# Performance work log

Hardware: AMD Instinct MI355X
Metric: run time of the kernel (lower is better)

## Reference

```python
import jax, jax.numpy as jnp
import numpy as np

DIM = 512
HID = 2048
L = 4
VOCAB = 32000
EPS = 1e-6
B, S = 2, 2048


def rmsnorm(x, w, eps=EPS):
    xf = x.astype(jnp.float32)
    n = xf * jax.lax.rsqrt(jnp.mean(xf * xf, axis=-1, keepdims=True) + eps)
    return n.astype(x.dtype) * w


def setup_inputs() -> dict:
    key = jax.random.key(0)
    ks = jax.random.split(key, 12)
    sd = 0.02
    tokens = jax.random.randint(ks[0], (B, S), 0, VOCAB)
    emb = jax.random.normal(ks[1], (VOCAB, DIM), jnp.float32) * sd  # tied out_proj.weight
    decay_norm_w = jnp.ones((L, DIM), jnp.float32)
    lambda_w = jax.random.normal(ks[2], (L, 1, DIM), jnp.float32) * sd
    quantity_w = jax.random.normal(ks[3], (L, DIM, DIM), jnp.float32) * sd
    gate_w = jax.random.normal(ks[4], (L, DIM, DIM), jnp.float32) * sd
    output_w = jax.random.normal(ks[5], (L, DIM, DIM), jnp.float32) * sd
    ffn_norm_w = jnp.ones((L, DIM), jnp.float32)
    w_h = jax.random.normal(ks[6], (L, HID, DIM), jnp.float32) * sd
    w_g = jax.random.normal(ks[7], (L, HID, DIM), jnp.float32) * sd
    w_o = jax.random.normal(ks[8], (L, DIM, HID), jnp.float32) * sd
    out_norm_w = jnp.ones((DIM,), jnp.float32)
    return dict(tokens=tokens, emb=emb, decay_norm_w=decay_norm_w, lambda_w=lambda_w,
                quantity_w=quantity_w, gate_w=gate_w, output_w=output_w,
                ffn_norm_w=ffn_norm_w, w_h=w_h, w_g=w_g, w_o=w_o, out_norm_w=out_norm_w)


def _ted_forward(tokens, emb, decay_norm_w, lambda_w, quantity_w, gate_w,
                 output_w, ffn_norm_w, w_h, w_g, w_o, out_norm_w):
    s = tokens.shape[-1]
    idx = jnp.arange(s, dtype=jnp.float32)
    # time[i,j] = relu(i - j) ; equivalent to ones.tril_(-1).cumsum_(-2)
    time = jnp.maximum(idx[:, None] - idx[None, :], 0.0)  # [S,S]
    causal = idx[:, None] >= idx[None, :]                 # tril mask incl. diag
    x = emb[tokens]  # [B,S,D]
    for l in range(L):
        h = rmsnorm(x, decay_norm_w[l])
        # negative lambdas: log(sigmoid(h @ W_l^T)) -> [B,S,1] -> [B,1,S]
        nl = jnp.swapaxes(jax.nn.log_sigmoid(h @ lambda_w[l].T), -1, -2)
        decay = jnp.where(causal, jnp.exp(nl * time), 0.0)  # [B,S,S]
        q = h @ quantity_w[l].T                             # [B,S,D]
        out = jnp.einsum('bst,btd->bsd', decay, q)
        x = x + (jax.nn.silu(out) @ output_w[l].T) * (h @ gate_w[l].T)
        f = rmsnorm(x, ffn_norm_w[l])
        x = x + ((f @ w_h[l].T) * jax.nn.silu(f @ w_g[l].T)) @ w_o[l].T
    return rmsnorm(x, out_norm_w) @ emb.T  # [B,S,V]


def reference(tokens, emb, decay_norm_w, lambda_w, quantity_w, gate_w,
              output_w, ffn_norm_w, w_h, w_g, w_o, out_norm_w):
    return _ted_forward(tokens, emb, decay_norm_w, lambda_w, quantity_w, gate_w,
                        output_w, ffn_norm_w, w_h, w_g, w_o, out_norm_w)
```

## Files before the change

### kernel.cpp

```cpp
#include <hip/hip_runtime.h>
#include <cstdint>
#include <cstddef>


typedef __bf16 bf16_t;
typedef __bf16 bf16x2 __attribute__((ext_vector_type(2)));
typedef __bf16 bf16x4 __attribute__((ext_vector_type(4)));
typedef __bf16 bf16x8 __attribute__((ext_vector_type(8)));
typedef float  f32x4  __attribute__((ext_vector_type(4)));

#define TED_DIM   512
#define TED_HID   2048
#define TED_L     4
#define TED_VOCAB 32000
#define TED_B     2
#define TED_S     2048
#define TED_ROWS  4096
#define LOG2E     1.44269504088896340736f

#define GLDS16(gp, lp)                                                  \
    __builtin_amdgcn_global_load_lds(                                   \
        (__attribute__((address_space(1))) void*)(gp),                  \
        (__attribute__((address_space(3))) void*)(lp), 16, 0, 0)

__global__ void cvt_kernel(const float* __restrict__ in, bf16_t* __restrict__ out, int n4)
{
    int i = blockIdx.x * blockDim.x + threadIdx.x;
    if (i < n4) {
        float4 v = ((const float4*)in)[i];
        bf16x4 o;
        o[0] = (bf16_t)v.x; o[1] = (bf16_t)v.y; o[2] = (bf16_t)v.z; o[3] = (bf16_t)v.w;
        ((bf16x4*)out)[i] = o;
    }
}

__global__ void embed_kernel(const int* __restrict__ tok, const float* __restrict__ emb,
                             float* __restrict__ x)
{
    int r = blockIdx.x;
    int t = threadIdx.x;
    int id = tok[r];
    float4 v = *(const float4*)&emb[(size_t)id * TED_DIM + t * 4];
    *(float4*)&x[(size_t)r * TED_DIM + t * 4] = v;
}

__global__ void rmsnorm_kernel(const float* __restrict__ x, const float* __restrict__ w,
                               const float* __restrict__ lam,
                               bf16_t* __restrict__ hout, float* __restrict__ nl2out)
{
    int row = blockIdx.x;
    int t = threadIdx.x;
    int lane = t & 63, wv = t >> 6;
    const float* xr = x + (size_t)row * TED_DIM;

    float2 v = *(const float2*)&xr[t * 2];
    float ss = v.x * v.x + v.y * v.y;
    #pragma unroll
    for (int off = 32; off; off >>= 1) ss += __shfl_down(ss, off, 64);

    __shared__ float red[4];
    __shared__ float sscale;
    if (lane == 0) red[wv] = ss;
    __syncthreads();
    if (t == 0) {
        float s = red[0] + red[1] + red[2] + red[3];
        sscale = rsqrtf(s * (1.0f / (float)TED_DIM) + 1e-6f);
    }
    __syncthreads();
    float scale = sscale;

    float2 wv2 = *(const float2*)&w[t * 2];
    float h0 = v.x * scale * wv2.x;
    float h1 = v.y * scale * wv2.y;
    bf16x2 hb; hb[0] = (bf16_t)h0; hb[1] = (bf16_t)h1;
    *(bf16x2*)&hout[(size_t)row * TED_DIM + t * 2] = hb;

    if (lam != nullptr) {
        float2 l2 = *(const float2*)&lam[t * 2];
        float p = h0 * l2.x + h1 * l2.y;
        #pragma unroll
        for (int off = 32; off; off >>= 1) p += __shfl_down(p, off, 64);
        if (lane == 0) red[wv] = p;
        __syncthreads();
        if (t == 0) {
            float z = red[0] + red[1] + red[2] + red[3];
            float nl = fminf(z, 0.0f) - log1pf(__expf(-fabsf(z)));
            nl2out[row] = nl * LOG2E;
        }
    }
}

enum { EPI_BF16 = 0, EPI_F32 = 1, EPI_GMUL_ADDX = 2, EPI_ADDX = 3, EPI_SILUMUL = 4 };

template <int BM, int BN, int EPI>
__global__ __launch_bounds__(256)
void gemm_bt(const bf16_t* __restrict__ A, const bf16_t* __restrict__ B,
             int M, int N, int K,
             float* __restrict__ outf, bf16_t* __restrict__ outb,
             const float* __restrict__ gmul, const bf16_t* __restrict__ umul,
             float* __restrict__ xres)
{
    constexpr int TM = BM / 32, TN = BN / 32;
    __shared__ __align__(16) bf16_t sA[BM * 32];
    __shared__ __align__(16) bf16_t sB[BN * 32];

    int t = threadIdx.x;
    int lane = t & 63, w = t >> 6;
    int quad = lane >> 4, l16 = lane & 15;
    int m0 = blockIdx.y * BM, n0 = blockIdx.x * BN;
    int wm = (w & 1) * (BM / 2), wn = (w >> 1) * (BN / 2);
    int srow = t >> 2, skc = t & 3;

    f32x4 acc[TM][TN] = {};

    for (int k0 = 0; k0 < K; k0 += 32) {
        #pragma unroll
        for (int i = 0; i < BM / 64; i++) {
            int r = i * 64 + srow;
            GLDS16(&A[(size_t)(m0 + r) * K + k0 + skc * 8], &sA[r * 32 + skc * 8]);
        }
        #pragma unroll
        for (int i = 0; i < BN / 64; i++) {
            int r = i * 64 + srow;
            GLDS16(&B[(size_t)(n0 + r) * K + k0 + skc * 8], &sB[r * 32 + skc * 8]);
        }
        __syncthreads();
        bf16x8 af[TM], bfr[TN];
        #pragma unroll
        for (int i = 0; i < TM; i++)
            af[i] = *(const bf16x8*)&sA[(wm + i * 16 + l16) * 32 + quad * 8];
        #pragma unroll
        for (int j = 0; j < TN; j++)
            bfr[j] = *(const bf16x8*)&sB[(wn + j * 16 + l16) * 32 + quad * 8];
        #pragma unroll
        for (int i = 0; i < TM; i++)
            #pragma unroll
            for (int j = 0; j < TN; j++)
                acc[i][j] = __builtin_amdgcn_mfma_f32_16x16x32_bf16(af[i], bfr[j], acc[i][j], 0, 0, 0);
        __syncthreads();
    }

    #pragma unroll
    for (int i = 0; i < TM; i++) {
        #pragma unroll
        for (int j = 0; j < TN; j++) {
            int col = n0 + wn + j * 16 + l16;
            #pragma unroll
            for (int r = 0; r < 4; r++) {
                int rowg = m0 + wm + i * 16 + quad * 4 + r;
                size_t idx = (size_t)rowg * N + col;
                float v = acc[i][j][r];
                if constexpr (EPI == EPI_BF16) {
                    outb[idx] = (bf16_t)v;
                } else if constexpr (EPI == EPI_F32) {
                    outf[idx] = v;
                } else if constexpr (EPI == EPI_GMUL_ADDX) {
                    xres[idx] += v * gmul[idx];
                } else if constexpr (EPI == EPI_ADDX) {
                    xres[idx] += v;
                } else {
                    float u = (float)umul[idx];
                    float s = v / (1.0f + __expf(-v));
                    outb[idx] = (bf16_t)(u * s);
                }
            }
        }
    }
}

template <int BM, int BN, int EPI>
static void launch_gemm(hipStream_t s, const bf16_t* A, const bf16_t* B,
                        int M, int N, int K,
                        float* outf = nullptr, bf16_t* outb = nullptr,
                        const float* gmul = nullptr, const bf16_t* umul = nullptr,
                        float* xres = nullptr)
{
    dim3 grid(N / BN, M / BM);
    gemm_bt<BM, BN, EPI><<<grid, 256, 0, s>>>(A, B, M, N, K, outf, outb, gmul, umul, xres);
}

__global__ __launch_bounds__(256)
void decay_kernel(const bf16_t* __restrict__ qT, const float* __restrict__ nl2,
                  bf16_t* __restrict__ aout)
{
    constexpr int BI = 64, BD = 128;
    __shared__ __align__(16) bf16_t sQ[BD * 32];

    int t = threadIdx.x;
    int lane = t & 63, w = t >> 6;
    int quad = lane >> 4, l16 = lane & 15;
    int d0 = blockIdx.x * BD;
    int i0 = blockIdx.y * BI;
    int b  = blockIdx.z;
    int wm = (w & 1) * 32, wn = (w >> 1) * 64;
    int srow = t >> 2, skc = t & 3;

    f32x4 acc[2][4] = {};

    int jt_end = i0 + BI;
    for (int j0 = 0; j0 < jt_end; j0 += 32) {
        #pragma unroll
        for (int i = 0; i < 2; i++) {
            int r = i * 64 + srow;
            GLDS16(&qT[(size_t)(d0 + r) * TED_ROWS + b * TED_S + j0 + skc * 8],
                   &sQ[r * 32 + skc * 8]);
        }
        float4 nA = *(const float4*)&nl2[b * TED_S + j0 + quad * 8];
        float4 nB = *(const float4*)&nl2[b * TED_S + j0 + quad * 8 + 4];
        float nn[8] = {nA.x, nA.y, nA.z, nA.w, nB.x, nB.y, nB.z, nB.w};
        bf16x8 af[2];
        #pragma unroll
        for (int i = 0; i < 2; i++) {
            int mi = i0 + wm + i * 16 + l16;
            #pragma unroll
            for (int jj = 0; jj < 8; jj++) {
                int j = j0 + quad * 8 + jj;
                int tt = mi - j;
                float dv = (tt >= 0) ? exp2f(nn[jj] * (float)tt) : 0.0f;
                af[i][jj] = (bf16_t)dv;
            }
        }
        __syncthreads();
        bf16x8 bfr[4];
        #pragma unroll
        for (int j = 0; j < 4; j++)
            bfr[j] = *(const bf16x8*)&sQ[(wn + j * 16 + l16) * 32 + quad * 8];
        #pragma unroll
        for (int i = 0; i < 2; i++)
            #pragma unroll
            for (int j = 0; j < 4; j++)
                acc[i][j] = __builtin_amdgcn_mfma_f32_16x16x32_bf16(af[i], bfr[j], acc[i][j], 0, 0, 0);
        __syncthreads();
    }

    #pragma unroll
    for (int i = 0; i < 2; i++) {
        #pragma unroll
        for (int j = 0; j < 4; j++) {
            int d = d0 + wn + j * 16 + l16;
            #pragma unroll
            for (int r = 0; r < 4; r++) {
                int ig = i0 + wm + i * 16 + quad * 4 + r;
                float v = acc[i][j][r];
                float s = v / (1.0f + __expf(-v));
                aout[(size_t)(b * TED_S + ig) * TED_DIM + d] = (bf16_t)s;
            }
        }
    }
}

extern "C" void kernel_launch(void* const* d_in, const int* in_sizes, int n_in,
                              void* d_out, int out_size, void* d_ws, size_t ws_size,
                              hipStream_t stream)
{
    const int*   tokens       = (const int*)d_in[0];
    const float* emb          = (const float*)d_in[1];
    const float* decay_norm_w = (const float*)d_in[2];
    const float* lambda_w     = (const float*)d_in[3];
    const float* quantity_w   = (const float*)d_in[4];
    const float* gate_w       = (const float*)d_in[5];
    const float* output_w     = (const float*)d_in[6];
    const float* ffn_norm_w   = (const float*)d_in[7];
    const float* w_h          = (const float*)d_in[8];
    const float* w_g          = (const float*)d_in[9];
    const float* w_o          = (const float*)d_in[10];
    const float* out_norm_w   = (const float*)d_in[11];

    constexpr int D = TED_DIM, H = TED_HID, L = TED_L, V = TED_VOCAB, R = TED_ROWS;

    char* ws = (char*)d_ws;
    size_t off = 0;
    auto alloc = [&](size_t bytes) -> char* {
        char* p = ws + off;
        off += (bytes + 255) & ~(size_t)255;
        return p;
    };
    bf16_t* emb_bf = (bf16_t*)alloc((size_t)V * D * 2);
    bf16_t* qw_bf  = (bf16_t*)alloc((size_t)L * D * D * 2);
    bf16_t* gw_bf  = (bf16_t*)alloc((size_t)L * D * D * 2);
    bf16_t* ow_bf  = (bf16_t*)alloc((size_t)L * D * D * 2);
    bf16_t* wh_bf  = (bf16_t*)alloc((size_t)L * H * D * 2);
    bf16_t* wg_bf  = (bf16_t*)alloc((size_t)L * H * D * 2);
    bf16_t* wo_bf  = (bf16_t*)alloc((size_t)L * D * H * 2);
    float*  x      = (float*)alloc((size_t)R * D * 4);
    bf16_t* h_bf   = (bf16_t*)alloc((size_t)R * D * 2);
    float*  nl2    = (float*)alloc((size_t)R * 4);
    bf16_t* qT_bf  = (bf16_t*)alloc((size_t)D * R * 2);
    float*  g_f32  = (float*)alloc((size_t)R * D * 4);
    bf16_t* a_bf   = (bf16_t*)alloc((size_t)R * D * 2);
    bf16_t* f_bf   = (bf16_t*)alloc((size_t)R * D * 2);
    bf16_t* u_bf   = (bf16_t*)alloc((size_t)R * H * 2);
    bf16_t* t_bf   = (bf16_t*)alloc((size_t)R * H * 2);
    if (off > ws_size) return;

    auto cvt = [&](const float* src, bf16_t* dst, size_t n) {
        int n4 = (int)(n / 4);
        cvt_kernel<<<dim3((n4 + 255) / 256), dim3(256), 0, stream>>>(src, dst, n4);
    };
    cvt(emb,        emb_bf, (size_t)V * D);
    cvt(quantity_w, qw_bf,  (size_t)L * D * D);
    cvt(gate_w,     gw_bf,  (size_t)L * D * D);
    cvt(output_w,   ow_bf,  (size_t)L * D * D);
    cvt(w_h,        wh_bf,  (size_t)L * H * D);
    cvt(w_g,        wg_bf,  (size_t)L * H * D);
    cvt(w_o,        wo_bf,  (size_t)L * D * H);

    embed_kernel<<<dim3(R), dim3(128), 0, stream>>>(tokens, emb, x);

    for (int l = 0; l < L; l++) {
        rmsnorm_kernel<<<dim3(R), dim3(256), 0, stream>>>(
            x, decay_norm_w + (size_t)l * D, lambda_w + (size_t)l * D, h_bf, nl2);
        launch_gemm<64, 64, EPI_F32>(stream, h_bf, gw_bf + (size_t)l * D * D, R, D, D, g_f32);
        launch_gemm<64, 64, EPI_BF16>(stream, qw_bf + (size_t)l * D * D, h_bf, D, R, D,
                                      nullptr, qT_bf);
        decay_kernel<<<dim3(D / 128, TED_S / 64, TED_B), dim3(256), 0, stream>>>(qT_bf, nl2, a_bf);
        launch_gemm<64, 64, EPI_GMUL_ADDX>(stream, a_bf, ow_bf + (size_t)l * D * D, R, D, D,
                                           nullptr, nullptr, g_f32, nullptr, x);
        rmsnorm_kernel<<<dim3(R), dim3(256), 0, stream>>>(
            x, ffn_norm_w + (size_t)l * D, nullptr, f_bf, nullptr);
        launch_gemm<128, 128, EPI_BF16>(stream, f_bf, wh_bf + (size_t)l * H * D, R, H, D,
                                        nullptr, u_bf);
        launch_gemm<128, 128, EPI_SILUMUL>(stream, f_bf, wg_bf + (size_t)l * H * D, R, H, D,
                                           nullptr, t_bf, nullptr, u_bf, nullptr);
        launch_gemm<64, 64, EPI_ADDX>(stream, t_bf, wo_bf + (size_t)l * D * H, R, D, H,
                                      nullptr, nullptr, nullptr, nullptr, x);
    }

    rmsnorm_kernel<<<dim3(R), dim3(256), 0, stream>>>(x, out_norm_w, nullptr, f_bf, nullptr);
    launch_gemm<128, 128, EPI_F32>(stream, f_bf, emb_bf, R, V, D, (float*)d_out);
}
```

Baseline: 1.518 ms.

## Fuse FFN up/gate GEMMs, swizzle LDS with K=64 tiles, batch conversions, warp-per-row rmsnorm

Several changes land together. The two FFN up-projection GEMMs are fused into one kernel that computes both products from a shared A tile and applies SiLU-multiply in its epilogue, which drops the u_bf intermediate and a second read of the activations. The generic GEMM now uses K=64 tiles with an XOR-swizzled LDS layout to cut bank conflicts and halve the number of barriers. The seven weight conversions are merged into one grid-stride launch, rmsnorm now handles one row per wavefront without shared-memory reductions, and the decay kernel is regrouped so each wave owns 16 rows and all 128 columns. The cost is a larger LDS footprint and register use per block, which may lower occupancy.

```diff
diff --git a/kernel.cpp b/kernel.cpp
--- a/kernel.cpp
+++ b/kernel.cpp
@@ -23,14 +23,24 @@
         (__attribute__((address_space(1))) void*)(gp),                  \
         (__attribute__((address_space(3))) void*)(lp), 16, 0, 0)
 
-__global__ void cvt_kernel(const float* __restrict__ in, bf16_t* __restrict__ out, int n4)
-{
-    int i = blockIdx.x * blockDim.x + threadIdx.x;
-    if (i < n4) {
-        float4 v = ((const float4*)in)[i];
-        bf16x4 o;
-        o[0] = (bf16_t)v.x; o[1] = (bf16_t)v.y; o[2] = (bf16_t)v.z; o[3] = (bf16_t)v.w;
-        ((bf16x4*)out)[i] = o;
+struct CvtSeg { const float* src; bf16_t* dst; int n4; };
+struct CvtArgs { CvtSeg seg[7]; };
+
+__global__ __launch_bounds__(256) void cvt_all_kernel(CvtArgs a)
+{
+    int i0 = blockIdx.x * blockDim.x + threadIdx.x;
+    int stride = gridDim.x * blockDim.x;
+    #pragma unroll 1
+    for (int s = 0; s < 7; s++) {
+        const float4* src = (const float4*)a.seg[s].src;
+        bf16x4* dst = (bf16x4*)a.seg[s].dst;
+        int n4 = a.seg[s].n4;
+        for (int i = i0; i < n4; i += stride) {
+            float4 v = src[i];
+            bf16x4 o;
+            o[0] = (bf16_t)v.x; o[1] = (bf16_t)v.y; o[2] = (bf16_t)v.z; o[3] = (bf16_t)v.w;
+            dst[i] = o;
+        }
     }
 }
 
@@ -44,99 +54,96 @@
     *(float4*)&x[(size_t)r * TED_DIM + t * 4] = v;
 }
 
-__global__ void rmsnorm_kernel(const float* __restrict__ x, const float* __restrict__ w,
-                               const float* __restrict__ lam,
-                               bf16_t* __restrict__ hout, float* __restrict__ nl2out)
-{
-    int row = blockIdx.x;
+__global__ __launch_bounds__(256)
+void rmsnorm_kernel(const float* __restrict__ x, const float* __restrict__ w,
+                    const float* __restrict__ lam,
+                    bf16_t* __restrict__ hout, float* __restrict__ nl2out)
+{
     int t = threadIdx.x;
     int lane = t & 63, wv = t >> 6;
+    int row = blockIdx.x * 4 + wv;
     const float* xr = x + (size_t)row * TED_DIM;
 
-    float2 v = *(const float2*)&xr[t * 2];
-    float ss = v.x * v.x + v.y * v.y;
-    #pragma unroll
-    for (int off = 32; off; off >>= 1) ss += __shfl_down(ss, off, 64);
-
-    __shared__ float red[4];
-    __shared__ float sscale;
-    if (lane == 0) red[wv] = ss;
-    __syncthreads();
-    if (t == 0) {
-        float s = red[0] + red[1] + red[2] + red[3];
-        sscale = rsqrtf(s * (1.0f / (float)TED_DIM) + 1e-6f);
-    }
-    __syncthreads();
-    float scale = sscale;
-
-    float2 wv2 = *(const float2*)&w[t * 2];
-    float h0 = v.x * scale * wv2.x;
-    float h1 = v.y * scale * wv2.y;
-    bf16x2 hb; hb[0] = (bf16_t)h0; hb[1] = (bf16_t)h1;
-    *(bf16x2*)&hout[(size_t)row * TED_DIM + t * 2] = hb;
+    float4 a = *(const float4*)&xr[lane * 8];
+    float4 b = *(const float4*)&xr[lane * 8 + 4];
+    float ss = a.x * a.x + a.y * a.y + a.z * a.z + a.w * a.w
+             + b.x * b.x + b.y * b.y + b.z * b.z + b.w * b.w;
+    #pragma unroll
+    for (int off = 32; off; off >>= 1) ss += __shfl_xor(ss, off, 64);
+    float scale = rsqrtf(ss * (1.0f / (float)TED_DIM) + 1e-6f);
+
+    float4 wa = *(const float4*)&w[lane * 8];
+    float4 wb = *(const float4*)&w[lane * 8 + 4];
+    float h[8] = { a.x * scale * wa.x, a.y * scale * wa.y, a.z * scale * wa.z, a.w * scale * wa.w,
+                   b.x * scale * wb.x, b.y * scale * wb.y, b.z * scale * wb.z, b.w * scale * wb.w };
+    bf16x8 hb;
+    #pragma unroll
+    for (int k = 0; k < 8; k++) hb[k] = (bf16_t)h[k];
+    *(bf16x8*)&hout[(size_t)row * TED_DIM + lane * 8] = hb;
 
     if (lam != nullptr) {
-        float2 l2 = *(const float2*)&lam[t * 2];
-        float p = h0 * l2.x + h1 * l2.y;
-        #pragma unroll
-        for (int off = 32; off; off >>= 1) p += __shfl_down(p, off, 64);
-        if (lane == 0) red[wv] = p;
-        __syncthreads();
-        if (t == 0) {
-            float z = red[0] + red[1] + red[2] + red[3];
-            float nl = fminf(z, 0.0f) - log1pf(__expf(-fabsf(z)));
+        float4 la = *(const float4*)&lam[lane * 8];
+        float4 lb = *(const float4*)&lam[lane * 8 + 4];
+        float p = h[0] * la.x + h[1] * la.y + h[2] * la.z + h[3] * la.w
+                + h[4] * lb.x + h[5] * lb.y + h[6] * lb.z + h[7] * lb.w;
+        #pragma unroll
+        for (int off = 32; off; off >>= 1) p += __shfl_xor(p, off, 64);
+        if (lane == 0) {
+            float nl = fminf(p, 0.0f) - log1pf(__expf(-fabsf(p)));
             nl2out[row] = nl * LOG2E;
         }
     }
 }
 
-enum { EPI_BF16 = 0, EPI_F32 = 1, EPI_GMUL_ADDX = 2, EPI_ADDX = 3, EPI_SILUMUL = 4 };
+enum { EPI_BF16 = 0, EPI_F32 = 1, EPI_GMUL_ADDX = 2, EPI_ADDX = 3 };
 
 template <int BM, int BN, int EPI>
 __global__ __launch_bounds__(256)
 void gemm_bt(const bf16_t* __restrict__ A, const bf16_t* __restrict__ B,
              int M, int N, int K,
              float* __restrict__ outf, bf16_t* __restrict__ outb,
-             const float* __restrict__ gmul, const bf16_t* __restrict__ umul,
-             float* __restrict__ xres)
+             const float* __restrict__ gmul, float* __restrict__ xres)
 {
     constexpr int TM = BM / 32, TN = BN / 32;
-    __shared__ __align__(16) bf16_t sA[BM * 32];
-    __shared__ __align__(16) bf16_t sB[BN * 32];
+    __shared__ __align__(16) bf16_t sA[BM * 64];
+    __shared__ __align__(16) bf16_t sB[BN * 64];
 
     int t = threadIdx.x;
     int lane = t & 63, w = t >> 6;
     int quad = lane >> 4, l16 = lane & 15;
     int m0 = blockIdx.y * BM, n0 = blockIdx.x * BN;
     int wm = (w & 1) * (BM / 2), wn = (w >> 1) * (BN / 2);
-    int srow = t >> 2, skc = t & 3;
+    int srow = t >> 3;
+    int skc  = (t & 7) ^ (srow & 7);
 
     f32x4 acc[TM][TN] = {};
 
-    for (int k0 = 0; k0 < K; k0 += 32) {
-        #pragma unroll
-        for (int i = 0; i < BM / 64; i++) {
-            int r = i * 64 + srow;
-            GLDS16(&A[(size_t)(m0 + r) * K + k0 + skc * 8], &sA[r * 32 + skc * 8]);
-        }
-        #pragma unroll
-        for (int i = 0; i < BN / 64; i++) {
-            int r = i * 64 + srow;
-            GLDS16(&B[(size_t)(n0 + r) * K + k0 + skc * 8], &sB[r * 32 + skc * 8]);
-        }
-        __syncthreads();
-        bf16x8 af[TM], bfr[TN];
-        #pragma unroll
-        for (int i = 0; i < TM; i++)
-            af[i] = *(const bf16x8*)&sA[(wm + i * 16 + l16) * 32 + quad * 8];
-        #pragma unroll
-        for (int j = 0; j < TN; j++)
-            bfr[j] = *(const bf16x8*)&sB[(wn + j * 16 + l16) * 32 + quad * 8];
-        #pragma unroll
-        for (int i = 0; i < TM; i++)
+    for (int k0 = 0; k0 < K; k0 += 64) {
+        #pragma unroll
+        for (int i = 0; i < BM / 32; i++)
+            GLDS16(&A[(size_t)(m0 + i * 32 + srow) * K + k0 + skc * 8],
+                   &sA[(i * 32 + srow) * 64 + (t & 7) * 8]);
+        #pragma unroll
+        for (int i = 0; i < BN / 32; i++)
+            GLDS16(&B[(size_t)(n0 + i * 32 + srow) * K + k0 + skc * 8],
+                   &sB[(i * 32 + srow) * 64 + (t & 7) * 8]);
+        __syncthreads();
+        #pragma unroll
+        for (int ks = 0; ks < 2; ks++) {
+            int csw = ((ks * 4 + quad) ^ (l16 & 7)) * 8;
+            bf16x8 af[TM], bfr[TN];
+            #pragma unroll
+            for (int i = 0; i < TM; i++)
+                af[i] = *(const bf16x8*)&sA[(wm + i * 16 + l16) * 64 + csw];
             #pragma unroll
             for (int j = 0; j < TN; j++)
-                acc[i][j] = __builtin_amdgcn_mfma_f32_16x16x32_bf16(af[i], bfr[j], acc[i][j], 0, 0, 0);
+                bfr[j] = *(const bf16x8*)&sB[(wn + j * 16 + l16) * 64 + csw];
+            #pragma unroll
+            for (int i = 0; i < TM; i++)
+                #pragma unroll
+                for (int j = 0; j < TN; j++)
+                    acc[i][j] = __builtin_amdgcn_mfma_f32_16x16x32_bf16(af[i], bfr[j], acc[i][j], 0, 0, 0);
+        }
         __syncthreads();
     }
 
@@ -156,12 +163,8 @@
                     outf[idx] = v;
                 } else if constexpr (EPI == EPI_GMUL_ADDX) {
                     xres[idx] += v * gmul[idx];
-                } else if constexpr (EPI == EPI_ADDX) {
+                } else {
                     xres[idx] += v;
-                } else {
-                    float u = (float)umul[idx];
-                    float s = v / (1.0f + __expf(-v));
-                    outb[idx] = (bf16_t)(u * s);
                 }
             }
         }
@@ -172,11 +175,83 @@
 static void launch_gemm(hipStream_t s, const bf16_t* A, const bf16_t* B,
                         int M, int N, int K,
                         float* outf = nullptr, bf16_t* outb = nullptr,
-                        const float* gmul = nullptr, const bf16_t* umul = nullptr,
-                        float* xres = nullptr)
+                        const float* gmul = nullptr, float* xres = nullptr)
 {
     dim3 grid(N / BN, M / BM);
-    gemm_bt<BM, BN, EPI><<<grid, 256, 0, s>>>(A, B, M, N, K, outf, outb, gmul, umul, xres);
+    gemm_bt<BM, BN, EPI><<<grid, 256, 0, s>>>(A, B, M, N, K, outf, outb, gmul, xres);
+}
+
+__global__ __launch_bounds__(256)
+void gemm_ffn(const bf16_t* __restrict__ A, const bf16_t* __restrict__ Bh,
+              const bf16_t* __restrict__ Bg, bf16_t* __restrict__ outb)
+{
+    constexpr int K = TED_DIM, N = TED_HID;
+    __shared__ __align__(16) bf16_t sA[128 * 64];
+    __shared__ __align__(16) bf16_t sH[64 * 64];
+    __shared__ __align__(16) bf16_t sG[64 * 64];
+
+    int t = threadIdx.x;
+    int lane = t & 63, w = t >> 6;
+    int quad = lane >> 4, l16 = lane & 15;
+    int m0 = blockIdx.y * 128, n0 = blockIdx.x * 64;
+    int wm = (w & 1) * 64, wn = (w >> 1) * 32;
+    int srow = t >> 3;
+    int skc  = (t & 7) ^ (srow & 7);
+
+    f32x4 aU[4][2] = {}, aV[4][2] = {};
+
+    for (int k0 = 0; k0 < K; k0 += 64) {
+        #pragma unroll
+        for (int i = 0; i < 4; i++)
+            GLDS16(&A[(size_t)(m0 + i * 32 + srow) * K + k0 + skc * 8],
+                   &sA[(i * 32 + srow) * 64 + (t & 7) * 8]);
+        #pragma unroll
+        for (int i = 0; i < 2; i++)
+            GLDS16(&Bh[(size_t)(n0 + i * 32 + srow) * K + k0 + skc * 8],
+                   &sH[(i * 32 + srow) * 64 + (t & 7) * 8]);
+        #pragma unroll
+        for (int i = 0; i < 2; i++)
+            GLDS16(&Bg[(size_t)(n0 + i * 32 + srow) * K + k0 + skc * 8],
+                   &sG[(i * 32 + srow) * 64 + (t & 7) * 8]);
+        __syncthreads();
+        #pragma unroll
+        for (int ks = 0; ks < 2; ks++) {
+            int csw = ((ks * 4 + quad) ^ (l16 & 7)) * 8;
+            bf16x8 af[4], bh[2], bg[2];
+            #pragma unroll
+            for (int i = 0; i < 4; i++)
+                af[i] = *(const bf16x8*)&sA[(wm + i * 16 + l16) * 64 + csw];
+            #pragma unroll
+            for (int j = 0; j < 2; j++) {
+                bh[j] = *(const bf16x8*)&sH[(wn + j * 16 + l16) * 64 + csw];
+                bg[j] = *(const bf16x8*)&sG[(wn + j * 16 + l16) * 64 + csw];
+            }
+            #pragma unroll
+            for (int i = 0; i < 4; i++) {
+                #pragma unroll
+                for (int j = 0; j < 2; j++) {
+                    aU[i][j] = __builtin_amdgcn_mfma_f32_16x16x32_bf16(af[i], bh[j], aU[i][j], 0, 0, 0);
+                    aV[i][j] = __builtin_amdgcn_mfma_f32_16x16x32_bf16(af[i], bg[j], aV[i][j], 0, 0, 0);
+                }
+            }
+        }
+        __syncthreads();
+    }
+
+    #pragma unroll
+    for (int i = 0; i < 4; i++) {
+        #pragma unroll
+        for (int j = 0; j < 2; j++) {
+            int col = n0 + wn + j * 16 + l16;
+            #pragma unroll
+            for (int r = 0; r < 4; r++) {
+                int rowg = m0 + wm + i * 16 + quad * 4 + r;
+                float u = aU[i][j][r], v = aV[i][j][r];
+                float s = v / (1.0f + __expf(-v));
+                outb[(size_t)rowg * N + col] = (bf16_t)(u * s);
+            }
+        }
+    }
 }
 
 __global__ __launch_bounds__(256)
@@ -192,59 +267,47 @@
     int d0 = blockIdx.x * BD;
     int i0 = blockIdx.y * BI;
     int b  = blockIdx.z;
-    int wm = (w & 1) * 32, wn = (w >> 1) * 64;
-    int srow = t >> 2, skc = t & 3;
-
-    f32x4 acc[2][4] = {};
-
-    int jt_end = i0 + BI;
-    for (int j0 = 0; j0 < jt_end; j0 += 32) {
-        #pragma unroll
-        for (int i = 0; i < 2; i++) {
-            int r = i * 64 + srow;
-            GLDS16(&qT[(size_t)(d0 + r) * TED_ROWS + b * TED_S + j0 + skc * 8],
-                   &sQ[r * 32 + skc * 8]);
-        }
+    int srow = t >> 2;
+    int skc  = (t & 3) ^ (srow & 3);
+
+    f32x4 acc[8] = {};
+    int mi = i0 + w * 16 + l16;
+
+    for (int j0 = 0; j0 < i0 + BI; j0 += 32) {
+        #pragma unroll
+        for (int i = 0; i < 2; i++)
+            GLDS16(&qT[(size_t)(d0 + i * 64 + srow) * TED_ROWS + b * TED_S + j0 + skc * 8],
+                   &sQ[(i * 64 + srow) * 32 + (t & 3) * 8]);
         float4 nA = *(const float4*)&nl2[b * TED_S + j0 + quad * 8];
         float4 nB = *(const float4*)&nl2[b * TED_S + j0 + quad * 8 + 4];
         float nn[8] = {nA.x, nA.y, nA.z, nA.w, nB.x, nB.y, nB.z, nB.w};
-        bf16x8 af[2];
-        #pragma unroll
-        for (int i = 0; i < 2; i++) {
-            int mi = i0 + wm + i * 16 + l16;
-            #pragma unroll
-            for (int jj = 0; jj < 8; jj++) {
-                int j = j0 + quad * 8 + jj;
-                int tt = mi - j;
-                float dv = (tt >= 0) ? exp2f(nn[jj] * (float)tt) : 0.0f;
-                af[i][jj] = (bf16_t)dv;
-            }
-        }
-        __syncthreads();
-        bf16x8 bfr[4];
-        #pragma unroll
-        for (int j = 0; j < 4; j++)
-            bfr[j] = *(const bf16x8*)&sQ[(wn + j * 16 + l16) * 32 + quad * 8];
-        #pragma unroll
-        for (int i = 0; i < 2; i++)
-            #pragma unroll
-            for (int j = 0; j < 4; j++)
-                acc[i][j] = __builtin_amdgcn_mfma_f32_16x16x32_bf16(af[i], bfr[j], acc[i][j], 0, 0, 0);
-        __syncthreads();
-    }
-
-    #pragma unroll
-    for (int i = 0; i < 2; i++) {
-        #pragma unroll
-        for (int j = 0; j < 4; j++) {
-            int d = d0 + wn + j * 16 + l16;
-            #pragma unroll
-            for (int r = 0; r < 4; r++) {
-                int ig = i0 + wm + i * 16 + quad * 4 + r;
-                float v = acc[i][j][r];
-                float s = v / (1.0f + __expf(-v));
-                aout[(size_t)(b * TED_S + ig) * TED_DIM + d] = (bf16_t)s;
-            }
+        bf16x8 af;
+        #pragma unroll
+        for (int jj = 0; jj < 8; jj++) {
+            int j = j0 + quad * 8 + jj;
+            int tt = mi - j;
+            float dv = (tt >= 0) ? exp2f(nn[jj] * (float)tt) : 0.0f;
+            af[jj] = (bf16_t)dv;
+        }
+        __syncthreads();
+        int cq = (quad ^ (l16 & 3)) * 8;
+        #pragma unroll
+        for (int j = 0; j < 8; j++) {
+            bf16x8 bfr = *(const bf16x8*)&sQ[(j * 16 + l16) * 32 + cq];
+            acc[j] = __builtin_amdgcn_mfma_f32_16x16x32_bf16(af, bfr, acc[j], 0, 0, 0);
+        }
+        __syncthreads();
+    }
+
+    #pragma unroll
+    for (int j = 0; j < 8; j++) {
+        int d = d0 + j * 16 + l16;
+        #pragma unroll
+        for (int r = 0; r < 4; r++) {
+            int ig = i0 + w * 16 + quad * 4 + r;
+            float v = acc[j][r];
+            float s = v / (1.0f + __expf(-v));
+            aout[(size_t)(b * TED_S + ig) * TED_DIM + d] = (bf16_t)s;
         }
     }
 }
@@ -289,43 +352,38 @@
     float*  g_f32  = (float*)alloc((size_t)R * D * 4);
     bf16_t* a_bf   = (bf16_t*)alloc((size_t)R * D * 2);
     bf16_t* f_bf   = (bf16_t*)alloc((size_t)R * D * 2);
-    bf16_t* u_bf   = (bf16_t*)alloc((size_t)R * H * 2);
     bf16_t* t_bf   = (bf16_t*)alloc((size_t)R * H * 2);
     if (off > ws_size) return;
 
-    auto cvt = [&](const float* src, bf16_t* dst, size_t n) {
-        int n4 = (int)(n / 4);
-        cvt_kernel<<<dim3((n4 + 255) / 256), dim3(256), 0, stream>>>(src, dst, n4);
-    };
-    cvt(emb,        emb_bf, (size_t)V * D);
-    cvt(quantity_w, qw_bf,  (size_t)L * D * D);
-    cvt(gate_w,     gw_bf,  (size_t)L * D * D);
-    cvt(output_w,   ow_bf,  (size_t)L * D * D);
-    cvt(w_h,        wh_bf,  (size_t)L * H * D);
-    cvt(w_g,        wg_bf,  (size_t)L * H * D);
-    cvt(w_o,        wo_bf,  (size_t)L * D * H);
+    CvtArgs ca;
+    ca.seg[0] = { emb,        emb_bf, (int)((size_t)V * D / 4) };
+    ca.seg[1] = { quantity_w, qw_bf,  (int)((size_t)L * D * D / 4) };
+    ca.seg[2] = { gate_w,     gw_bf,  (int)((size_t)L * D * D / 4) };
+    ca.seg[3] = { output_w,   ow_bf,  (int)((size_t)L * D * D / 4) };
+    ca.seg[4] = { w_h,        wh_bf,  (int)((size_t)L * H * D / 4) };
+    ca.seg[5] = { w_g,        wg_bf,  (int)((size_t)L * H * D / 4) };
+    ca.seg[6] = { w_o,        wo_bf,  (int)((size_t)L * D * H / 4) };
+    cvt_all_kernel<<<dim3(2048), dim3(256), 0, stream>>>(ca);
 
     embed_kernel<<<dim3(R), dim3(128), 0, stream>>>(tokens, emb, x);
 
     for (int l = 0; l < L; l++) {
-        rmsnorm_kernel<<<dim3(R), dim3(256), 0, stream>>>(
+        rmsnorm_kernel<<<dim3(R / 4), dim3(256), 0, stream>>>(
             x, decay_norm_w + (size_t)l * D, lambda_w + (size_t)l * D, h_bf, nl2);
         launch_gemm<64, 64, EPI_F32>(stream, h_bf, gw_bf + (size_t)l * D * D, R, D, D, g_f32);
         launch_gemm<64, 64, EPI_BF16>(stream, qw_bf + (size_t)l * D * D, h_bf, D, R, D,
                                       nullptr, qT_bf);
         decay_kernel<<<dim3(D / 128, TED_S / 64, TED_B), dim3(256), 0, stream>>>(qT_bf, nl2, a_bf);
         launch_gemm<64, 64, EPI_GMUL_ADDX>(stream, a_bf, ow_bf + (size_t)l * D * D, R, D, D,
-                                           nullptr, nullptr, g_f32, nullptr, x);
-        rmsnorm_kernel<<<dim3(R), dim3(256), 0, stream>>>(
+                                           nullptr, nullptr, g_f32, x);
+        rmsnorm_kernel<<<dim3(R / 4), dim3(256), 0, stream>>>(
             x, ffn_norm_w + (size_t)l * D, nullptr, f_bf, nullptr);
-        launch_gemm<128, 128, EPI_BF16>(stream, f_bf, wh_bf + (size_t)l * H * D, R, H, D,
-                                        nullptr, u_bf);
-        launch_gemm<128, 128, EPI_SILUMUL>(stream, f_bf, wg_bf + (size_t)l * H * D, R, H, D,
-                                           nullptr, t_bf, nullptr, u_bf, nullptr);
+        gemm_ffn<<<dim3(H / 64, R / 128), dim3(256), 0, stream>>>(
+            f_bf, wh_bf + (size_t)l * H * D, wg_bf + (size_t)l * H * D, t_bf);
         launch_gemm<64, 64, EPI_ADDX>(stream, t_bf, wo_bf + (size_t)l * D * H, R, D, H,
-                                      nullptr, nullptr, nullptr, nullptr, x);
-    }
-
-    rmsnorm_kernel<<<dim3(R), dim3(256), 0, stream>>>(x, out_norm_w, nullptr, f_bf, nullptr);
+                                      nullptr, nullptr, nullptr, x);
+    }
+
+    rmsnorm_kernel<<<dim3(R / 4), dim3(256), 0, stream>>>(x, out_norm_w, nullptr, f_bf, nullptr);
     launch_gemm<128, 128, EPI_F32>(stream, f_bf, emb_bf, R, V, D, (float*)d_out);
 }
```

Measured after the change: 1.381 ms. -9.0%, faster.
